# Kernel optimization log

Hardware: AMD Instinct MI355X
Metric: run time of the kernel (lower is better)

Reference implementation:

```python
import math
import jax, jax.numpy as jnp
import numpy as np

# dims (from init_kwargs / forward signature)
B, N, K = 8, 1024, 8            # batch, nodes, num_neighbors
NC, TED, TEC = 64, 128, 64      # num_channels, time_embedding_dim, time_embedding_channels
C = NC + TEC                    # model dim = 128
H, Dh = 8, 16                   # heads, dim_head
HD = H * Dh
L = 4                           # num_layers
RH = 32                         # radial-net hidden width
NPATH = 10                      # radial scalars: k00,k10,k01,k11a,k11b,v00,v10,v01,v11a,v11b


def _g(k, shape, fan_in):
    return jax.random.normal(k, shape, dtype=jnp.float32) / np.sqrt(float(fan_in))


def setup_inputs() -> dict:
    key = jax.random.key(0)
    ks = jax.random.split(key, 16)
    return dict(
        x=jax.random.normal(ks[0], (B, N, 3), dtype=jnp.float32),
        y=jax.random.normal(ks[1], (B, N, 3), dtype=jnp.float32),
        t=jax.random.uniform(ks[2], (B,), dtype=jnp.float32) * 1000.0,
        Wt1=_g(ks[3], (TED, TED), TED), bt1=jnp.zeros((TED,), jnp.float32),
        Wt2=_g(ks[4], (TED, TEC), TED), bt2=jnp.zeros((TEC,), jnp.float32),
        Win0=_g(ks[5], (TEC + 3, C), TEC + 3), bin0=jnp.zeros((C,), jnp.float32),
        Win1=_g(ks[6], (1, C), 1),
        Wqkv=_g(ks[7], (L, 12, C, HD), C),           # q0,q1,k00,k10,k01,k11a,k11b,v00,v10,v01,v11a,v11b
        Wr1=_g(ks[8], (L, 1, RH), 1), br1=jnp.zeros((L, RH), jnp.float32),
        Wr2=_g(ks[9], (L, RH, H * NPATH), RH), br2=jnp.zeros((L, H * NPATH), jnp.float32),
        Wo=_g(ks[10], (L, 2, HD, C), HD), bo=jnp.zeros((L, 2, C), jnp.float32),
        Wout=_g(ks[11], (3, C), C), bout=jnp.zeros((3,), jnp.float32),
    )


def _forward(x, y, t, Wt1, bt1, Wt2, bt2, Win0, bin0, Win1, Wqkv,
             Wr1, br1, Wr2, br2, Wo, bo, Wout, bout):
    b, n = x.shape[0], x.shape[1]
    # sinusoidal time embedding + time MLP
    half = TED // 2
    freqs = jnp.exp(-math.log(10000.0) * jnp.arange(half, dtype=x.dtype) / half)
    emb = t[:, None] * freqs
    temb = jnp.concatenate([jnp.sin(emb), jnp.cos(emb)], axis=-1)          # [B,TED]
    temb = jax.nn.silu(temb @ Wt1 + bt1) @ Wt2 + bt2                        # [B,TEC]

    # degree-0 input = [time_embed | coords], degree-1 input = coords (1 channel)
    deg0 = jnp.concatenate([jnp.broadcast_to(temb[:, None, :], (b, n, TEC)), x], axis=-1)
    f0 = deg0 @ Win0 + bin0                                                 # [B,N,C]
    f1 = jnp.einsum('bnv,c->bncv', x, Win1[0])                              # [B,N,C,3]

    # k-nearest-neighbor graph on coordinates (shared across layers)
    d2 = jnp.sum((x[:, :, None, :] - x[:, None, :, :]) ** 2, axis=-1)       # [B,N,N]
    d2 = d2 + jnp.eye(n, dtype=x.dtype) * 1e9                               # exclude self
    _, idx = jax.lax.top_k(-d2, K)                                          # [B,N,K]
    gather = lambda f: jax.vmap(lambda a, i: a[i])(f, idx)                  # [B,N,...] -> [B,N,K,...]
    rel = gather(x) - x[:, :, None, :]                                      # [B,N,K,3]
    r = jnp.sqrt(jnp.sum(rel ** 2, axis=-1, keepdims=True) + 1e-8)          # [B,N,K,1]
    rhat = rel / r

    inv_scale = 1.0 / float(np.sqrt(2 * Dh))
    for l in range(L):
        Wl = Wqkv[l].reshape(12, C, H, Dh)
        q0 = jnp.einsum('bnc,chd->bnhd', f0, Wl[0])
        q1 = jnp.einsum('bncv,chd->bnhdv', f1, Wl[1])
        f0j, f1j = gather(f0), gather(f1)                                   # [B,N,K,C], [B,N,K,C,3]
        # radial network -> per-head, per-path scalars
        Rn = (jax.nn.silu(r @ Wr1[l] + br1[l]) @ Wr2[l] + br2[l]).reshape(b, n, K, H, NPATH)
        # equivariant tensor-product paths (degrees 0/1, spherical harmonics Y0,Y1,Y2)
        dot1 = jnp.einsum('bnkcv,bnkv->bnkc', f1j, rhat)                    # 1->0 path
        sym = 3.0 * dot1[..., None] * rhat[:, :, :, None, :] - f1j          # Y2 (traceless sym) 1->1 path
        p0 = lambda f, w: jnp.einsum('bnkc,chd->bnkhd', f, w)
        p1 = lambda f, w: jnp.einsum('bnkcv,chd->bnkhdv', f, w)
        rh = rhat[:, :, :, None, None, :]
        k0 = p0(f0j, Wl[2]) * Rn[..., 0:1] + p0(dot1, Wl[3]) * Rn[..., 1:2]
        k1 = (p0(f0j, Wl[4])[..., None] * rh * Rn[..., 2][..., None, None]
              + p1(f1j, Wl[5]) * Rn[..., 3][..., None, None]
              + p1(sym, Wl[6]) * Rn[..., 4][..., None, None])
        v0 = p0(f0j, Wl[7]) * Rn[..., 5:6] + p0(dot1, Wl[8]) * Rn[..., 6:7]
        v1 = (p0(f0j, Wl[9])[..., None] * rh * Rn[..., 7][..., None, None]
              + p1(f1j, Wl[10]) * Rn[..., 8][..., None, None]
              + p1(sym, Wl[11]) * Rn[..., 9][..., None, None])
        logits = (jnp.einsum('bnhd,bnkhd->bnhk', q0, k0)
                  + jnp.einsum('bnhdv,bnkhdv->bnhk', q1, k1)) * inv_scale
        attn = jax.nn.softmax(logits, axis=-1)
        o0 = jnp.einsum('bnhk,bnkhd->bnhd', attn, v0).reshape(b, n, HD)
        o1 = jnp.einsum('bnhk,bnkhdv->bnhdv', attn, v1).reshape(b, n, HD, 3)
        f0 = f0 + o0 @ Wo[l, 0] + bo[l, 0]
        f1 = f1 + jnp.einsum('bnev,ec->bncv', o1, Wo[l, 1]) + bo[l, 1][None, None, :, None]

    # output layer Linear(dim, 3) applied as per-component channel mixing on the type-1 output
    return jnp.einsum('bncv,vc->bnv', f1, Wout) + bout                      # [B,N,3]


def reference(x, y, t, Wt1, bt1, Wt2, bt2, Win0, bin0, Win1, Wqkv,
              Wr1, br1, Wr2, br2, Wo, bo, Wout, bout):
    return _forward(x, y, t, Wt1, bt1, Wt2, bt2, Win0, bin0, Win1, Wqkv,
                    Wr1, br1, Wr2, br2, Wo, bo, Wout, bout)
```

## Files before the change

### kernel.cpp

```cpp
#include <hip/hip_runtime.h>
#include <math.h>

#define NBATCH 8
#define NPTS   1024
#define KNN    8
#define CC     128
#define HD_    128
#define TED_   128
#define TEC_   64
#define RH     32
#define NL     4

typedef _Float16 half8 __attribute__((ext_vector_type(8)));
typedef _Float16 h4v  __attribute__((ext_vector_type(4)));
typedef float f32x4 __attribute__((ext_vector_type(4)));

__device__ __forceinline__ unsigned long long shflxor_u64(unsigned long long v, int m) {
  return (unsigned long long)__shfl_xor((long long)v, m, 8);
}

__global__ __launch_bounds__(128) void k_temb(
    const float* __restrict__ t, const float* __restrict__ Wt1,
    const float* __restrict__ bt1, const float* __restrict__ Wt2,
    const float* __restrict__ bt2, const float* __restrict__ Win0,
    const float* __restrict__ bin0, float* __restrict__ pre0)
{
  int b = blockIdx.x;
  int tid = threadIdx.x;
  __shared__ float e128[TED_];
  __shared__ float h1[TED_];
  __shared__ float te[TEC_];
  float tv = t[b];
  if (tid < 64) {
    float fr = expf((-9.210340371976184f * (float)tid) * 0.015625f);
    float em = tv * fr;
    e128[tid]      = sinf(em);
    e128[tid + 64] = cosf(em);
  }
  __syncthreads();
  {
    float acc = bt1[tid];
    for (int i = 0; i < TED_; ++i) acc += e128[i] * Wt1[i * TED_ + tid];
    h1[tid] = acc / (1.0f + expf(-acc));
  }
  __syncthreads();
  if (tid < TEC_) {
    float acc = bt2[tid];
    for (int j = 0; j < TED_; ++j) acc += h1[j] * Wt2[j * TEC_ + tid];
    te[tid] = acc;
  }
  __syncthreads();
  {
    float acc = bin0[tid];
    for (int i = 0; i < TEC_; ++i) acc += te[i] * Win0[i * CC + tid];
    pre0[b * CC + tid] = acc;
  }
}

__global__ __launch_bounds__(256) void k_init(
    const float* __restrict__ x, const float* __restrict__ Win0,
    const float* __restrict__ Win1, const float* __restrict__ pre0,
    float* __restrict__ f0, float* __restrict__ f1,
    _Float16* __restrict__ f0h, _Float16* __restrict__ f1h)
{
  int node = blockIdx.x * 2 + (threadIdx.x >> 7);
  int c = threadIdx.x & 127;
  int b = node >> 10;
  float x0 = x[node * 3 + 0], x1 = x[node * 3 + 1], x2 = x[node * 3 + 2];
  float acc = pre0[b * CC + c]
            + x0 * Win0[(TEC_ + 0) * CC + c]
            + x1 * Win0[(TEC_ + 1) * CC + c]
            + x2 * Win0[(TEC_ + 2) * CC + c];
  f0[(size_t)node * CC + c] = acc;
  f0h[(size_t)node * CC + c] = (_Float16)acc;
  float w1 = Win1[c];
  float v0 = x0 * w1, v1 = x1 * w1, v2 = x2 * w1;
  f1[((size_t)node * 3 + 0) * CC + c] = v0;
  f1[((size_t)node * 3 + 1) * CC + c] = v1;
  f1[((size_t)node * 3 + 2) * CC + c] = v2;
  f1h[((size_t)node * 3 + 0) * CC + c] = (_Float16)v0;
  f1h[((size_t)node * 3 + 1) * CC + c] = (_Float16)v1;
  f1h[((size_t)node * 3 + 2) * CC + c] = (_Float16)v2;
}

__global__ __launch_bounds__(256) void k_knn(
    const float* __restrict__ x, int* __restrict__ idx,
    float* __restrict__ rhat, float* __restrict__ rl)
{
  const int b    = blockIdx.x >> 5;
  const int tile = blockIdx.x & 31;
  const int tid  = threadIdx.x;
  const int qg   = tid >> 3;
  const int sub  = tid & 7;

  __shared__ float xsx[NPTS], xsy[NPTS], xsz[NPTS];

  for (int i = tid; i < NPTS; i += 256) {
    const float* xp = x + ((size_t)b * NPTS + i) * 3;
    xsx[i] = xp[0]; xsy[i] = xp[1]; xsz[i] = xp[2];
  }
  __syncthreads();

  const int n = tile * 32 + qg;
  const float qx = xsx[n], qy = xsy[n], qz = xsz[n];

  unsigned long long bd[KNN];
  #pragma unroll
  for (int k = 0; k < KNN; ++k) bd[k] = ~0ull;

  const int j0 = sub * 128;
  const int ph = sub * 4;
  for (int it = 0; it < 128; ++it) {
    int j = j0 + ((it + ph) & 127);
    float dx = qx - xsx[j];
    float dy = qy - xsy[j];
    float dz = qz - xsz[j];
    float s = __fadd_rn(__fadd_rn(__fmul_rn(dx, dx), __fmul_rn(dy, dy)),
                        __fmul_rn(dz, dz));
    if (j == n) s = 1.0e9f;
    unsigned long long key =
        ((unsigned long long)__float_as_uint(s) << 32) | (unsigned int)j;
    if (key < bd[KNN - 1]) {
      bd[KNN - 1] = key;
      #pragma unroll
      for (int q = KNN - 1; q > 0; --q) {
        if (bd[q] < bd[q - 1]) {
          unsigned long long tmp = bd[q]; bd[q] = bd[q - 1]; bd[q - 1] = tmp;
        }
      }
    }
  }

  unsigned long long res[KNN];
  #pragma unroll
  for (int r = 0; r < KNN; ++r) {
    unsigned long long m = bd[0];
    unsigned long long o;
    o = shflxor_u64(m, 1); m = (o < m) ? o : m;
    o = shflxor_u64(m, 2); m = (o < m) ? o : m;
    o = shflxor_u64(m, 4); m = (o < m) ? o : m;
    if (bd[0] == m) {
      #pragma unroll
      for (int q = 0; q < KNN - 1; ++q) bd[q] = bd[q + 1];
      bd[KNN - 1] = ~0ull;
    }
    res[r] = m;
  }

  unsigned long long key = res[0];
  #pragma unroll
  for (int r = 1; r < KNN; ++r) if (sub == r) key = res[r];
  int j = (int)(key & 0xffffffffu);
  size_t base = ((size_t)b * NPTS + n) * KNN + sub;
  idx[base] = j;
  float rx = xsx[j] - qx;
  float ry = xsy[j] - qy;
  float rz = xsz[j] - qz;
  float rr2 = rx * rx + ry * ry + rz * rz + 1e-8f;
  float r = sqrtf(rr2);
  rl[base] = r;
  rhat[base * 3 + 0] = rx / r;
  rhat[base * 3 + 1] = ry / r;
  rhat[base * 3 + 2] = rz / r;
}

__global__ __launch_bounds__(256) void k_wconv(
    const float* __restrict__ Wqkv, const float* __restrict__ Wo,
    _Float16* __restrict__ Whq, _Float16* __restrict__ Who)
{
  __shared__ _Float16 T[128][136];
  int m = blockIdx.x;
  const float* src; _Float16* dst;
  if (m < 48) { src = Wqkv + (size_t)m * 16384; dst = Whq + (size_t)m * 16384; }
  else { src = Wo + (size_t)(m - 48) * 16384; dst = Who + (size_t)(m - 48) * 16384; }
  int tid = threadIdx.x;
  for (int i = tid; i < 16384; i += 256) {
    int k = i >> 7, n = i & 127;
    T[n][k] = (_Float16)src[i];
  }
  __syncthreads();
  for (int i = tid; i < 16384; i += 256) {
    int n = i >> 7, k = i & 127;
    dst[i] = T[n][k];
  }
}

#define MFMA_BODY(A_, ROWBASE_, WT_)                                          \
  const int tid  = threadIdx.x;                                               \
  const int lane = tid & 63;                                                  \
  const int w    = tid >> 6;                                                  \
  const int r15  = lane & 15;                                                 \
  const int g    = lane >> 4;                                                 \
  half8 bf[2][4];                                                             \
  _Pragma("unroll")                                                           \
  for (int ntl = 0; ntl < 2; ++ntl) {                                         \
    int n = (w * 2 + ntl) * 16 + r15;                                         \
    const _Float16* wp = (WT_) + (size_t)n * 128 + g * 8;                     \
    _Pragma("unroll")                                                         \
    for (int ks = 0; ks < 4; ++ks)                                            \
      bf[ntl][ks] = *(const half8*)(wp + ks * 32);                            \
  }                                                                           \
  {                                                                           \
    int r = tid >> 1;                                                         \
    const _Float16* src = (A_) + (size_t)((ROWBASE_) + r) * 128;              \
    int c0 = (tid & 1) * 8;                                                   \
    _Pragma("unroll")                                                         \
    for (int q = 0; q < 8; ++q) {                                             \
      int c = c0 + q;                                                         \
      *(uint4*)&As[r][c * 8] = *(const uint4*)(src + c * 8);                  \
    }                                                                         \
  }                                                                           \
  __syncthreads();                                                            \
  f32x4 acc[8][2] = {};                                                       \
  _Pragma("unroll")                                                           \
  for (int ks = 0; ks < 4; ++ks) {                                            \
    half8 a[8];                                                               \
    _Pragma("unroll")                                                         \
    for (int mt = 0; mt < 8; ++mt)                                            \
      a[mt] = *(const half8*)&As[mt * 16 + r15][ks * 32 + g * 8];             \
    _Pragma("unroll")                                                         \
    for (int mt = 0; mt < 8; ++mt) {                                          \
      acc[mt][0] = __builtin_amdgcn_mfma_f32_16x16x32_f16(a[mt], bf[0][ks], acc[mt][0], 0, 0, 0); \
      acc[mt][1] = __builtin_amdgcn_mfma_f32_16x16x32_f16(a[mt], bf[1][ks], acc[mt][1], 0, 0, 0); \
    }                                                                         \
  }

__global__ __launch_bounds__(256) void k_proj_mfma(
    const _Float16* __restrict__ f0h, const _Float16* __restrict__ f1h,
    const _Float16* __restrict__ Wh, _Float16* __restrict__ P0,
    _Float16* __restrict__ P1, int nb0)
{
  __shared__ _Float16 As[128][136];
  int z = blockIdx.x;
  const _Float16* A; const _Float16* Wt; _Float16* P; int ldP, colBase, rowBase;
  if (z < nb0 * 5) {
    const int map0[5] = {0, 2, 4, 7, 9};
    int m = z / nb0, rb = z - m * nb0;
    A = f0h; rowBase = rb * 128;
    Wt = Wh + (size_t)map0[m] * 16384;
    P = P0; ldP = 640; colBase = m * 128;
  } else {
    z -= nb0 * 5;
    int nb1 = nb0 * 3;
    const int map1[7] = {1, 3, 5, 6, 8, 10, 11};
    int m = z / nb1, rb = z - m * nb1;
    A = f1h; rowBase = rb * 128;
    Wt = Wh + (size_t)map1[m] * 16384;
    P = P1; ldP = 896; colBase = m * 128;
  }
  MFMA_BODY(A, rowBase, Wt)
  #pragma unroll
  for (int mt = 0; mt < 8; ++mt) {
    #pragma unroll
    for (int ntl = 0; ntl < 2; ++ntl) {
      int col = colBase + (w * 2 + ntl) * 16 + r15;
      #pragma unroll
      for (int i = 0; i < 4; ++i) {
        int r = rowBase + mt * 16 + g * 4 + i;
        P[(size_t)r * ldP + col] = (_Float16)acc[mt][ntl][i];
      }
    }
  }
}

__global__ __launch_bounds__(256) void k_wo_mfma(
    const _Float16* __restrict__ o0h, const _Float16* __restrict__ o1h,
    const _Float16* __restrict__ Who_l, const float* __restrict__ bo_l,
    float* __restrict__ f0, float* __restrict__ f1,
    _Float16* __restrict__ f0h, _Float16* __restrict__ f1h, int nb0)
{
  __shared__ _Float16 As[128][136];
  int z = blockIdx.x;
  const _Float16* A; const _Float16* Wt; const float* bias;
  float* F; _Float16* FH; int rowBase;
  if (z < nb0) {
    A = o0h; Wt = Who_l; bias = bo_l; F = f0; FH = f0h; rowBase = z * 128;
  } else {
    z -= nb0;
    A = o1h; Wt = Who_l + 16384; bias = bo_l + CC; F = f1; FH = f1h; rowBase = z * 128;
  }
  MFMA_BODY(A, rowBase, Wt)
  #pragma unroll
  for (int mt = 0; mt < 8; ++mt) {
    #pragma unroll
    for (int ntl = 0; ntl < 2; ++ntl) {
      int col = (w * 2 + ntl) * 16 + r15;
      float bv = bias[col];
      #pragma unroll
      for (int i = 0; i < 4; ++i) {
        int r = rowBase + mt * 16 + g * 4 + i;
        size_t p = (size_t)r * 128 + col;
        float val = F[p] + acc[mt][ntl][i] + bv;
        F[p] = val;
        FH[p] = (_Float16)val;
      }
    }
  }
}

__global__ __launch_bounds__(256) void k_attn(
    const _Float16* __restrict__ P0, const _Float16* __restrict__ P1,
    const int* __restrict__ idx, const float* __restrict__ rhat,
    const float* __restrict__ rl,
    const float* __restrict__ Wr1, const float* __restrict__ br1,
    const float* __restrict__ Wr2, const float* __restrict__ br2,
    _Float16* __restrict__ o0h, _Float16* __restrict__ o1h,
    int nodeBase, int layer, int nbg)
{
  const int t = threadIdx.x;
  const int wv = t >> 5;
  const int lane = t & 31;
  const int z = blockIdx.x;
  const int bb = z % nbg;
  const int qbase = (z / nbg) * 8;
  const int nodeLocal = bb * NPTS + qbase + wv;
  const int node = nodeBase + nodeLocal;
  const int batchRow = bb * NPTS;

  __shared__ float rn_s[8][KNN][80];
  __shared__ float hid_s[8][KNN][RH];
  __shared__ float rh_s[8][KNN][3];
  __shared__ float rl_s[8][KNN];

  {
    int f = t;
    if (f < 192) {
      int nd = f / 24, e = f % 24;
      rh_s[nd][e / 3][e % 3] =
          rhat[((size_t)(nodeBase + bb * NPTS + qbase + nd)) * KNN * 3 + e];
    } else {
      int f2 = f - 192;
      int nd = f2 >> 3, k = f2 & 7;
      rl_s[nd][k] = rl[((size_t)(nodeBase + bb * NPTS + qbase + nd)) * KNN + k];
    }
  }
  __syncthreads();

  const float* wr1 = Wr1 + layer * RH;
  const float* wb1 = br1 + layer * RH;
  #pragma unroll
  for (int u = 0; u < 8; ++u) {
    int f = u * 256 + t;
    int nd = f >> 8, k = (f >> 5) & 7, i = f & 31;
    float zv = rl_s[nd][k] * wr1[i] + wb1[i];
    hid_s[nd][k][i] = zv / (1.0f + expf(-zv));
  }
  __syncthreads();
  const float* wr2 = Wr2 + layer * RH * 80;
  const float* wb2 = br2 + layer * 80;
  #pragma unroll
  for (int u = 0; u < 20; ++u) {
    int f = u * 256 + t;
    int nd = f / 640, rem = f - nd * 640;
    int k = rem / 80, col = rem - k * 80;
    float acc = wb2[col];
    #pragma unroll
    for (int i = 0; i < RH; ++i) acc += hid_s[nd][k][i] * wr2[i * 80 + col];
    rn_s[nd][k][col] = acc;
  }
  __syncthreads();

  const int c0 = lane * 4;
  const int h = lane >> 2;
  const _Float16* p0n = P0 + (size_t)nodeLocal * 640 + c0;
  const _Float16* p1n = P1 + (size_t)nodeLocal * 2688 + c0;
  h4v q0v  = *(const h4v*)(p0n);
  h4v q1xv = *(const h4v*)(p1n);
  h4v q1yv = *(const h4v*)(p1n + 896);
  h4v q1zv = *(const h4v*)(p1n + 1792);

  const float inv_scale = 0.17677669529663687f;
  const int* idxp = idx + (size_t)node * KNN;
  int jls[KNN];
  #pragma unroll
  for (int k = 0; k < KNN; ++k) jls[k] = batchRow + idxp[k];

  float m = -3.0e38f, ssum = 0.0f;
  float a0[4] = {}, ax[4] = {}, ay[4] = {}, az[4] = {};

  for (int k = 0; k < KNN; ++k) {
    int jl = jls[k];
    const _Float16* g0 = P0 + (size_t)jl * 640 + c0;
    const _Float16* g1 = P1 + (size_t)jl * 2688 + c0;
    float rx = rh_s[wv][k][0], ry = rh_s[wv][k][1], rz = rh_s[wv][k][2];

    h4v G02 = *(const h4v*)(g0 + 128), G04 = *(const h4v*)(g0 + 256);
    h4v G07 = *(const h4v*)(g0 + 384), G09 = *(const h4v*)(g0 + 512);
    h4v G13x = *(const h4v*)(g1 + 128),  G13y = *(const h4v*)(g1 + 896 + 128),  G13z = *(const h4v*)(g1 + 1792 + 128);
    h4v G15x = *(const h4v*)(g1 + 256),  G15y = *(const h4v*)(g1 + 896 + 256),  G15z = *(const h4v*)(g1 + 1792 + 256);
    h4v G16x = *(const h4v*)(g1 + 384),  G16y = *(const h4v*)(g1 + 896 + 384),  G16z = *(const h4v*)(g1 + 1792 + 384);
    h4v G18x = *(const h4v*)(g1 + 512),  G18y = *(const h4v*)(g1 + 896 + 512),  G18z = *(const h4v*)(g1 + 1792 + 512);
    h4v G1Ax = *(const h4v*)(g1 + 640),  G1Ay = *(const h4v*)(g1 + 896 + 640),  G1Az = *(const h4v*)(g1 + 1792 + 640);
    h4v G1Bx = *(const h4v*)(g1 + 768),  G1By = *(const h4v*)(g1 + 896 + 768),  G1Bz = *(const h4v*)(g1 + 1792 + 768);

    const float* rnh = &rn_s[wv][k][h * 10];
    float r0 = rnh[0], r1 = rnh[1], r2 = rnh[2], r3 = rnh[3], r4 = rnh[4];
    float r5 = rnh[5], r6 = rnh[6], r7 = rnh[7], r8 = rnh[8], r9 = rnh[9];

    float pl = 0.0f;
    float v0c[4], vxc[4], vyc[4], vzc[4];
    #pragma unroll
    for (int ci = 0; ci < 4; ++ci) {
      float g02 = (float)G02[ci], g04 = (float)G04[ci];
      float g07 = (float)G07[ci], g09 = (float)G09[ci];
      float g13x = (float)G13x[ci], g13y = (float)G13y[ci], g13z = (float)G13z[ci];
      float g15x = (float)G15x[ci], g15y = (float)G15y[ci], g15z = (float)G15z[ci];
      float g16x = (float)G16x[ci], g16y = (float)G16y[ci], g16z = (float)G16z[ci];
      float g18x = (float)G18x[ci], g18y = (float)G18y[ci], g18z = (float)G18z[ci];
      float g1ax = (float)G1Ax[ci], g1ay = (float)G1Ay[ci], g1az = (float)G1Az[ci];
      float g1bx = (float)G1Bx[ci], g1by = (float)G1By[ci], g1bz = (float)G1Bz[ci];

      float DP3 = g13x * rx + g13y * ry + g13z * rz;
      float DP6 = g16x * rx + g16y * ry + g16z * rz;
      float DP8 = g18x * rx + g18y * ry + g18z * rz;
      float DPB = g1bx * rx + g1by * ry + g1bz * rz;

      float k0  = g02 * r0 + DP3 * r1;
      float k1x = g04 * rx * r2 + g15x * r3 + (3.0f * rx * DP6 - g16x) * r4;
      float k1y = g04 * ry * r2 + g15y * r3 + (3.0f * ry * DP6 - g16y) * r4;
      float k1z = g04 * rz * r2 + g15z * r3 + (3.0f * rz * DP6 - g16z) * r4;
      v0c[ci] = g07 * r5 + DP8 * r6;
      vxc[ci] = g09 * rx * r7 + g1ax * r8 + (3.0f * rx * DPB - g1bx) * r9;
      vyc[ci] = g09 * ry * r7 + g1ay * r8 + (3.0f * ry * DPB - g1by) * r9;
      vzc[ci] = g09 * rz * r7 + g1az * r8 + (3.0f * rz * DPB - g1bz) * r9;

      pl += (float)q0v[ci] * k0 + (float)q1xv[ci] * k1x
          + (float)q1yv[ci] * k1y + (float)q1zv[ci] * k1z;
    }
    pl += __shfl_xor(pl, 1, 4);
    pl += __shfl_xor(pl, 2, 4);
    pl *= inv_scale;

    float mnew = fmaxf(m, pl);
    float scale = expf(m - mnew);
    float wgt = expf(pl - mnew);
    ssum = ssum * scale + wgt;
    #pragma unroll
    for (int ci = 0; ci < 4; ++ci) {
      a0[ci] = a0[ci] * scale + wgt * v0c[ci];
      ax[ci] = ax[ci] * scale + wgt * vxc[ci];
      ay[ci] = ay[ci] * scale + wgt * vyc[ci];
      az[ci] = az[ci] * scale + wgt * vzc[ci];
    }
    m = mnew;
  }

  float invs = 1.0f / ssum;
  h4v o;
  #pragma unroll
  for (int ci = 0; ci < 4; ++ci) o[ci] = (_Float16)(a0[ci] * invs);
  *(h4v*)(o0h + (size_t)nodeLocal * 128 + c0) = o;
  #pragma unroll
  for (int ci = 0; ci < 4; ++ci) o[ci] = (_Float16)(ax[ci] * invs);
  *(h4v*)(o1h + ((size_t)nodeLocal * 3 + 0) * 128 + c0) = o;
  #pragma unroll
  for (int ci = 0; ci < 4; ++ci) o[ci] = (_Float16)(ay[ci] * invs);
  *(h4v*)(o1h + ((size_t)nodeLocal * 3 + 1) * 128 + c0) = o;
  #pragma unroll
  for (int ci = 0; ci < 4; ++ci) o[ci] = (_Float16)(az[ci] * invs);
  *(h4v*)(o1h + ((size_t)nodeLocal * 3 + 2) * 128 + c0) = o;
}

__global__ __launch_bounds__(256) void k_out(
    const float* __restrict__ f1, const float* __restrict__ Wout,
    const float* __restrict__ bout, float* __restrict__ out)
{
  int i = blockIdx.x * 256 + threadIdx.x;
  int v = i % 3;
  const float* row = f1 + (size_t)i * CC;
  const float* w = Wout + v * CC;
  float acc = 0.0f;
  #pragma unroll
  for (int c = 0; c < CC; c += 4) {
    float4 fv = *(const float4*)&row[c];
    float4 wv = *(const float4*)&w[c];
    acc += fv.x * wv.x + fv.y * wv.y + fv.z * wv.z + fv.w * wv.w;
  }
  out[i] = acc + bout[v];
}

extern "C" void kernel_launch(void* const* d_in, const int* in_sizes, int n_in,
                              void* d_out, int out_size, void* d_ws, size_t ws_size,
                              hipStream_t stream) {
  const float* x    = (const float*)d_in[0];
  const float* t    = (const float*)d_in[2];
  const float* Wt1  = (const float*)d_in[3];
  const float* bt1  = (const float*)d_in[4];
  const float* Wt2  = (const float*)d_in[5];
  const float* bt2  = (const float*)d_in[6];
  const float* Win0 = (const float*)d_in[7];
  const float* bin0 = (const float*)d_in[8];
  const float* Win1 = (const float*)d_in[9];
  const float* Wqkv = (const float*)d_in[10];
  const float* Wr1  = (const float*)d_in[11];
  const float* br1  = (const float*)d_in[12];
  const float* Wr2  = (const float*)d_in[13];
  const float* br2  = (const float*)d_in[14];
  const float* Wo   = (const float*)d_in[15];
  const float* bo   = (const float*)d_in[16];
  const float* Wout = (const float*)d_in[17];
  const float* bout = (const float*)d_in[18];
  float* out = (float*)d_out;

  char* wsb = (char*)d_ws;
  size_t off = 0;
  auto alloc = [&](size_t bytes) -> void* {
    void* p = wsb + off;
    off = (off + bytes + 255) & ~(size_t)255;
    return p;
  };
  const int totalNodes = NBATCH * NPTS;
  float* pre0 = (float*)alloc((size_t)NBATCH * CC * 4);
  float* f0   = (float*)alloc((size_t)totalNodes * CC * 4);
  float* f1   = (float*)alloc((size_t)totalNodes * 3 * CC * 4);
  _Float16* f0h = (_Float16*)alloc((size_t)totalNodes * CC * 2);
  _Float16* f1h = (_Float16*)alloc((size_t)totalNodes * 3 * CC * 2);
  _Float16* Whq = (_Float16*)alloc((size_t)NL * 12 * CC * HD_ * 2);
  _Float16* Who = (_Float16*)alloc((size_t)NL * 2 * CC * HD_ * 2);
  int*   idx  = (int*)alloc((size_t)totalNodes * KNN * 4);
  float* rhat = (float*)alloc((size_t)totalNodes * KNN * 3 * 4);
  float* rl   = (float*)alloc((size_t)totalNodes * KNN * 4);
  size_t fixedBytes = off;
  size_t perBatch = (size_t)NPTS * ((640 + 2688) * 2 + (128 + 384) * 2);
  int nbg = 8;
  while (nbg > 1 && fixedBytes + (size_t)nbg * perBatch + 8192 > ws_size) nbg >>= 1;
  _Float16* P0  = (_Float16*)alloc((size_t)nbg * NPTS * 640 * 2);
  _Float16* P1  = (_Float16*)alloc((size_t)nbg * NPTS * 2688 * 2);
  _Float16* o0h = (_Float16*)alloc((size_t)nbg * NPTS * 128 * 2);
  _Float16* o1h = (_Float16*)alloc((size_t)nbg * NPTS * 384 * 2);

  k_temb<<<NBATCH, 128, 0, stream>>>(t, Wt1, bt1, Wt2, bt2, Win0, bin0, pre0);
  k_init<<<totalNodes / 2, 256, 0, stream>>>(x, Win0, Win1, pre0, f0, f1, f0h, f1h);
  k_knn<<<NBATCH * 32, 256, 0, stream>>>(x, idx, rhat, rl);
  k_wconv<<<56, 256, 0, stream>>>(Wqkv, Wo, Whq, Who);

  for (int g = 0; g < NBATCH / nbg; ++g) {
    int nodeBase = g * nbg * NPTS;
    int nodes = nbg * NPTS;
    int nb0 = nodes / 128;
    for (int l = 0; l < NL; ++l) {
      k_proj_mfma<<<nb0 * 26, 256, 0, stream>>>(
          f0h + (size_t)nodeBase * CC, f1h + (size_t)nodeBase * 3 * CC,
          Whq + (size_t)l * 12 * CC * HD_, P0, P1, nb0);
      k_attn<<<nodes / 8, 256, 0, stream>>>(
          P0, P1, idx, rhat, rl, Wr1, br1, Wr2, br2, o0h, o1h, nodeBase, l, nbg);
      k_wo_mfma<<<nb0 * 4, 256, 0, stream>>>(
          o0h, o1h, Who + (size_t)l * 2 * CC * HD_, bo + (size_t)(l * 2) * CC,
          f0 + (size_t)nodeBase * CC, f1 + (size_t)nodeBase * 3 * CC,
          f0h + (size_t)nodeBase * CC, f1h + (size_t)nodeBase * 3 * CC, nb0);
    }
  }
  k_out<<<(totalNodes * 3) / 256, 256, 0, stream>>>(f1, Wout, bout, out);
}
```

Measured before the change: 463.9 us.

## Precompute radial net for all layers in one kernel and split neighbors across half-waves

The radial MLP evaluation moves out of the per-layer attention kernel into a single upfront kernel that writes fp16 radial scalars for all layers. The attention kernel then reads these per head and gives each node a 64-lane wave, with two halves each handling four neighbors. The halves merge their partial online-softmax states through cross-lane shuffles. This removes redundant shared-memory MLP work and barriers from attention and doubles the thread parallelism per node, at the cost of extra global traffic for the Rn buffer (about 67MB written and read) and fp16 rounding of the radial scalars.

```diff
diff --git a/kernel.cpp b/kernel.cpp
--- a/kernel.cpp
+++ b/kernel.cpp
@@ -162,6 +162,52 @@
   rhat[base * 3 + 0] = rx / r;
   rhat[base * 3 + 1] = ry / r;
   rhat[base * 3 + 2] = rz / r;
+}
+
+__global__ __launch_bounds__(256) void k_rn(
+    const float* __restrict__ rl, const float* __restrict__ Wr1,
+    const float* __restrict__ br1, const float* __restrict__ Wr2,
+    const float* __restrict__ br2, _Float16* __restrict__ Rn)
+{
+  const int l = blockIdx.y;
+  const int e0 = blockIdx.x * 64;
+  const int t = threadIdx.x;
+  __shared__ float rls[64];
+  __shared__ float hid[64][33];
+  __shared__ float wsm[RH * 80];
+  if (t < 64) rls[t] = rl[e0 + t];
+  {
+    const float* wr2 = Wr2 + l * RH * 80;
+    for (int i = t; i < RH * 80; i += 256) wsm[i] = wr2[i];
+  }
+  __syncthreads();
+  {
+    const float* wr1 = Wr1 + l * RH;
+    const float* wb1 = br1 + l * RH;
+    int e = t >> 2, ib = (t & 3) * 8;
+    float rv = rls[e];
+    #pragma unroll
+    for (int q = 0; q < 8; ++q) {
+      int i = ib + q;
+      float zv = rv * wr1[i] + wb1[i];
+      hid[e][i] = zv / (1.0f + expf(-zv));
+    }
+  }
+  __syncthreads();
+  {
+    const float* wb2 = br2 + l * 80;
+    int e = t >> 2, cg = t & 3;
+    _Float16* dst = Rn + (((size_t)l * 65536) + e0 + e) * 128;
+    #pragma unroll
+    for (int q = 0; q < 20; ++q) {
+      int col = cg * 20 + q;
+      float acc = wb2[col];
+      #pragma unroll
+      for (int i = 0; i < RH; ++i) acc += hid[e][i] * wsm[i * 80 + col];
+      int hh = col / 10, j = col - hh * 10;
+      dst[hh * 16 + j] = (_Float16)acc;
+    }
+  }
 }
 
 __global__ __launch_bounds__(256) void k_wconv(
@@ -301,67 +347,32 @@
 __global__ __launch_bounds__(256) void k_attn(
     const _Float16* __restrict__ P0, const _Float16* __restrict__ P1,
     const int* __restrict__ idx, const float* __restrict__ rhat,
-    const float* __restrict__ rl,
-    const float* __restrict__ Wr1, const float* __restrict__ br1,
-    const float* __restrict__ Wr2, const float* __restrict__ br2,
+    const _Float16* __restrict__ RnL,
     _Float16* __restrict__ o0h, _Float16* __restrict__ o1h,
-    int nodeBase, int layer, int nbg)
+    int nodeBase, int nbg)
 {
   const int t = threadIdx.x;
-  const int wv = t >> 5;
-  const int lane = t & 31;
+  const int wv = t >> 6;
+  const int lane = t & 63;
+  const int cl = lane & 31;
+  const int nh = lane >> 5;
   const int z = blockIdx.x;
   const int bb = z % nbg;
-  const int qbase = (z / nbg) * 8;
+  const int qbase = (z / nbg) * 4;
   const int nodeLocal = bb * NPTS + qbase + wv;
   const int node = nodeBase + nodeLocal;
   const int batchRow = bb * NPTS;
 
-  __shared__ float rn_s[8][KNN][80];
-  __shared__ float hid_s[8][KNN][RH];
-  __shared__ float rh_s[8][KNN][3];
-  __shared__ float rl_s[8][KNN];
-
-  {
-    int f = t;
-    if (f < 192) {
-      int nd = f / 24, e = f % 24;
-      rh_s[nd][e / 3][e % 3] =
-          rhat[((size_t)(nodeBase + bb * NPTS + qbase + nd)) * KNN * 3 + e];
-    } else {
-      int f2 = f - 192;
-      int nd = f2 >> 3, k = f2 & 7;
-      rl_s[nd][k] = rl[((size_t)(nodeBase + bb * NPTS + qbase + nd)) * KNN + k];
-    }
-  }
-  __syncthreads();
-
-  const float* wr1 = Wr1 + layer * RH;
-  const float* wb1 = br1 + layer * RH;
-  #pragma unroll
-  for (int u = 0; u < 8; ++u) {
-    int f = u * 256 + t;
-    int nd = f >> 8, k = (f >> 5) & 7, i = f & 31;
-    float zv = rl_s[nd][k] * wr1[i] + wb1[i];
-    hid_s[nd][k][i] = zv / (1.0f + expf(-zv));
-  }
-  __syncthreads();
-  const float* wr2 = Wr2 + layer * RH * 80;
-  const float* wb2 = br2 + layer * 80;
-  #pragma unroll
-  for (int u = 0; u < 20; ++u) {
-    int f = u * 256 + t;
-    int nd = f / 640, rem = f - nd * 640;
-    int k = rem / 80, col = rem - k * 80;
-    float acc = wb2[col];
-    #pragma unroll
-    for (int i = 0; i < RH; ++i) acc += hid_s[nd][k][i] * wr2[i * 80 + col];
-    rn_s[nd][k][col] = acc;
-  }
-  __syncthreads();
-
-  const int c0 = lane * 4;
-  const int h = lane >> 2;
+  __shared__ float rh_s[4][KNN][3];
+  if (t < 96) {
+    int nd = t / 24, e = t % 24;
+    rh_s[nd][e / 3][e % 3] =
+        rhat[((size_t)(nodeBase + bb * NPTS + qbase + nd)) * KNN * 3 + e];
+  }
+  __syncthreads();
+
+  const int c0 = cl * 4;
+  const int h = cl >> 2;
   const _Float16* p0n = P0 + (size_t)nodeLocal * 640 + c0;
   const _Float16* p1n = P1 + (size_t)nodeLocal * 2688 + c0;
   h4v q0v  = *(const h4v*)(p0n);
@@ -370,19 +381,21 @@
   h4v q1zv = *(const h4v*)(p1n + 1792);
 
   const float inv_scale = 0.17677669529663687f;
-  const int* idxp = idx + (size_t)node * KNN;
-  int jls[KNN];
-  #pragma unroll
-  for (int k = 0; k < KNN; ++k) jls[k] = batchRow + idxp[k];
+  const int* idxp = idx + (size_t)node * KNN + nh * 4;
+  int jls[4];
+  #pragma unroll
+  for (int k = 0; k < 4; ++k) jls[k] = batchRow + idxp[k];
+  const _Float16* rnp = RnL + ((size_t)node * KNN + nh * 4) * 128 + h * 16;
 
   float m = -3.0e38f, ssum = 0.0f;
   float a0[4] = {}, ax[4] = {}, ay[4] = {}, az[4] = {};
 
-  for (int k = 0; k < KNN; ++k) {
+  for (int k = 0; k < 4; ++k) {
+    int kk = nh * 4 + k;
     int jl = jls[k];
     const _Float16* g0 = P0 + (size_t)jl * 640 + c0;
     const _Float16* g1 = P1 + (size_t)jl * 2688 + c0;
-    float rx = rh_s[wv][k][0], ry = rh_s[wv][k][1], rz = rh_s[wv][k][2];
+    float rx = rh_s[wv][kk][0], ry = rh_s[wv][kk][1], rz = rh_s[wv][kk][2];
 
     h4v G02 = *(const h4v*)(g0 + 128), G04 = *(const h4v*)(g0 + 256);
     h4v G07 = *(const h4v*)(g0 + 384), G09 = *(const h4v*)(g0 + 512);
@@ -393,9 +406,11 @@
     h4v G1Ax = *(const h4v*)(g1 + 640),  G1Ay = *(const h4v*)(g1 + 896 + 640),  G1Az = *(const h4v*)(g1 + 1792 + 640);
     h4v G1Bx = *(const h4v*)(g1 + 768),  G1By = *(const h4v*)(g1 + 896 + 768),  G1Bz = *(const h4v*)(g1 + 1792 + 768);
 
-    const float* rnh = &rn_s[wv][k][h * 10];
-    float r0 = rnh[0], r1 = rnh[1], r2 = rnh[2], r3 = rnh[3], r4 = rnh[4];
-    float r5 = rnh[5], r6 = rnh[6], r7 = rnh[7], r8 = rnh[8], r9 = rnh[9];
+    half8 rv = *(const half8*)(rnp + (size_t)k * 128);
+    h4v rv2 = *(const h4v*)(rnp + (size_t)k * 128 + 8);
+    float r0 = (float)rv[0], r1 = (float)rv[1], r2 = (float)rv[2], r3 = (float)rv[3];
+    float r4 = (float)rv[4], r5 = (float)rv[5], r6 = (float)rv[6], r7 = (float)rv[7];
+    float r8 = (float)rv2[0], r9 = (float)rv2[1];
 
     float pl = 0.0f;
     float v0c[4], vxc[4], vyc[4], vzc[4];
@@ -445,20 +460,42 @@
     m = mnew;
   }
 
-  float invs = 1.0f / ssum;
-  h4v o;
-  #pragma unroll
-  for (int ci = 0; ci < 4; ++ci) o[ci] = (_Float16)(a0[ci] * invs);
-  *(h4v*)(o0h + (size_t)nodeLocal * 128 + c0) = o;
-  #pragma unroll
-  for (int ci = 0; ci < 4; ++ci) o[ci] = (_Float16)(ax[ci] * invs);
-  *(h4v*)(o1h + ((size_t)nodeLocal * 3 + 0) * 128 + c0) = o;
-  #pragma unroll
-  for (int ci = 0; ci < 4; ++ci) o[ci] = (_Float16)(ay[ci] * invs);
-  *(h4v*)(o1h + ((size_t)nodeLocal * 3 + 1) * 128 + c0) = o;
-  #pragma unroll
-  for (int ci = 0; ci < 4; ++ci) o[ci] = (_Float16)(az[ci] * invs);
-  *(h4v*)(o1h + ((size_t)nodeLocal * 3 + 2) * 128 + c0) = o;
+  {
+    float mo = __shfl_xor(m, 32, 64);
+    float so = __shfl_xor(ssum, 32, 64);
+    float mn = fmaxf(m, mo);
+    float s_self = expf(m - mn);
+    float s_oth  = expf(mo - mn);
+    ssum = ssum * s_self + so * s_oth;
+    #pragma unroll
+    for (int ci = 0; ci < 4; ++ci) {
+      float o0 = __shfl_xor(a0[ci], 32, 64);
+      float ox = __shfl_xor(ax[ci], 32, 64);
+      float oy = __shfl_xor(ay[ci], 32, 64);
+      float oz = __shfl_xor(az[ci], 32, 64);
+      a0[ci] = a0[ci] * s_self + o0 * s_oth;
+      ax[ci] = ax[ci] * s_self + ox * s_oth;
+      ay[ci] = ay[ci] * s_self + oy * s_oth;
+      az[ci] = az[ci] * s_self + oz * s_oth;
+    }
+  }
+
+  if (nh == 0) {
+    float invs = 1.0f / ssum;
+    h4v o;
+    #pragma unroll
+    for (int ci = 0; ci < 4; ++ci) o[ci] = (_Float16)(a0[ci] * invs);
+    *(h4v*)(o0h + (size_t)nodeLocal * 128 + c0) = o;
+    #pragma unroll
+    for (int ci = 0; ci < 4; ++ci) o[ci] = (_Float16)(ax[ci] * invs);
+    *(h4v*)(o1h + ((size_t)nodeLocal * 3 + 0) * 128 + c0) = o;
+    #pragma unroll
+    for (int ci = 0; ci < 4; ++ci) o[ci] = (_Float16)(ay[ci] * invs);
+    *(h4v*)(o1h + ((size_t)nodeLocal * 3 + 1) * 128 + c0) = o;
+    #pragma unroll
+    for (int ci = 0; ci < 4; ++ci) o[ci] = (_Float16)(az[ci] * invs);
+    *(h4v*)(o1h + ((size_t)nodeLocal * 3 + 2) * 128 + c0) = o;
+  }
 }
 
 __global__ __launch_bounds__(256) void k_out(
@@ -520,6 +557,7 @@
   int*   idx  = (int*)alloc((size_t)totalNodes * KNN * 4);
   float* rhat = (float*)alloc((size_t)totalNodes * KNN * 3 * 4);
   float* rl   = (float*)alloc((size_t)totalNodes * KNN * 4);
+  _Float16* Rn = (_Float16*)alloc((size_t)NL * totalNodes * KNN * 128 * 2);
   size_t fixedBytes = off;
   size_t perBatch = (size_t)NPTS * ((640 + 2688) * 2 + (128 + 384) * 2);
   int nbg = 8;
@@ -533,6 +571,7 @@
   k_init<<<totalNodes / 2, 256, 0, stream>>>(x, Win0, Win1, pre0, f0, f1, f0h, f1h);
   k_knn<<<NBATCH * 32, 256, 0, stream>>>(x, idx, rhat, rl);
   k_wconv<<<56, 256, 0, stream>>>(Wqkv, Wo, Whq, Who);
+  k_rn<<<dim3(totalNodes * KNN / 64, NL), 256, 0, stream>>>(rl, Wr1, br1, Wr2, br2, Rn);
 
   for (int g = 0; g < NBATCH / nbg; ++g) {
     int nodeBase = g * nbg * NPTS;
@@ -542,8 +581,9 @@
       k_proj_mfma<<<nb0 * 26, 256, 0, stream>>>(
           f0h + (size_t)nodeBase * CC, f1h + (size_t)nodeBase * 3 * CC,
           Whq + (size_t)l * 12 * CC * HD_, P0, P1, nb0);
-      k_attn<<<nodes / 8, 256, 0, stream>>>(
-          P0, P1, idx, rhat, rl, Wr1, br1, Wr2, br2, o0h, o1h, nodeBase, l, nbg);
+      k_attn<<<nodes / 4, 256, 0, stream>>>(
+          P0, P1, idx, rhat, Rn + (size_t)l * totalNodes * KNN * 128,
+          o0h, o1h, nodeBase, nbg);
       k_wo_mfma<<<nb0 * 4, 256, 0, stream>>>(
           o0h, o1h, Who + (size_t)l * 2 * CC * HD_, bo + (size_t)(l * 2) * CC,
           f0 + (size_t)nodeBase * CC, f1 + (size_t)nodeBase * 3 * CC,
```

Result: slower. 542.5 us (+16.9%).
